# Performance work log

Hardware: AMD Instinct MI355X
Metric: run time of the kernel (lower is better)

## Reference

```python
import jax, jax.numpy as jnp
import numpy as np

START_TAG = 0
END_TAG = 63
NEG_INF = -10000.0


def setup_inputs() -> dict:
    key = jax.random.key(0)
    k1, k2, k3 = jax.random.split(key, 3)
    S, D, L = 32768, 1024, 64  # seq_len, feature_dim, num_labels
    feats = jax.random.normal(k1, (S, D), jnp.float32)
    W = jax.random.normal(k2, (L, D), jnp.float32) * 0.02  # nn.Linear weight [out,in]
    b = jnp.zeros((L,), jnp.float32)
    transitions = jax.random.normal(k3, (L, L), jnp.float32)
    transitions = transitions.at[START_TAG, :].set(NEG_INF).at[:, END_TAG].set(NEG_INF)
    return {"feats": feats, "W": W, "b": b, "transitions": transitions}


def reference(feats, W, b, transitions):
    # emissions: [S, L]
    emissions = feats @ W.T + b

    # Viterbi forward pass.  scores[j] after step t = best path score ending in label j.
    init_scores = transitions[:, START_TAG] + emissions[0]

    def step(scores, emit):
        # swt[j, i] = scores[i] + T[j, i]  (transition i -> j)
        swt = scores[None, :] + transitions  # [L, L]
        new_scores = emit + jnp.max(swt, axis=-1)
        back_ptr = jnp.argmax(swt, axis=-1)
        return new_scores, back_ptr

    final_scores, back_ptrs = jax.lax.scan(step, init_scores, emissions[1:])
    final_scores = final_scores + transitions[END_TAG]

    viterbi_score = jnp.max(final_scores)
    last_tag = jnp.argmax(final_scores)

    # Backtrack: tag[t-1] = back_ptrs[t-1][tag[t]] (back_ptrs[k] is for time k+1).
    def back(tag, bp):
        return bp[tag], tag

    first_tag, rest_tags = jax.lax.scan(back, last_tag, back_ptrs, reverse=True)
    tag_seq = jnp.concatenate([first_tag[None], rest_tags])  # [S]
    return viterbi_score, tag_seq
```

## Files before the change

kernel.cpp:

```cpp
#include <hip/hip_runtime.h>

#define S_LEN 32768
#define D_DIM 1024
#define L_LAB 64
#define LC 32
#define NCH (S_LEN / LC)
#define H_WARM 12
#define NSUP 32
#define SUPC 32

#define EM_OFF   0
#define BP_OFF   (S_LEN * 64 * 4)
#define MAPS_OFF (BP_OFF + S_LEN * 64)
#define BND_OFF  (MAPS_OFF + NCH * 64)
#define WIN_OFF  (BND_OFF + 1024)
#define END_OFF  (WIN_OFF + NCH * 4)
#define FIN_OFF  (END_OFF + NCH * 4)
#define WBF_OFF  (FIN_OFF + 256)

typedef __attribute__((ext_vector_type(8))) short short8;
typedef __attribute__((ext_vector_type(4))) float floatx4;

__device__ inline unsigned short f32_bf16_rne(float f) {
    unsigned v = __float_as_uint(f);
    v += 0x7FFFu + ((v >> 16) & 1u);
    return (unsigned short)(v >> 16);
}
__device__ inline unsigned umax(unsigned a, unsigned b) { return a > b ? a : b; }

__global__ __launch_bounds__(256) void wconv_kernel(
        const float* __restrict__ W, unsigned short* __restrict__ Wbf) {
    int i = blockIdx.x * 256 + threadIdx.x;
    Wbf[i] = f32_bf16_rne(W[i]);
}

__global__ __launch_bounds__(256) __attribute__((amdgpu_waves_per_eu(2, 2)))
void emis_kernel(
        const float* __restrict__ feats, const unsigned short* __restrict__ Wbf,
        const float* __restrict__ bvec, float* __restrict__ em) {
    __shared__ __align__(16) unsigned short As[64 * 72];
    __shared__ __align__(16) unsigned short Bs[64 * 72];

    const int tid = threadIdx.x;
    const int lan = tid & 15;
    const int q   = (tid >> 4) & 3;
    const int w   = tid >> 6;
    const int row0 = blockIdx.x * 64;

    floatx4 acc[4];
#pragma unroll
    for (int nt = 0; nt < 4; ++nt) acc[nt] = (floatx4){0.f, 0.f, 0.f, 0.f};

    for (int kb = 0; kb < D_DIM; kb += 64) {
        __syncthreads();
#pragma unroll
        for (int i = 0; i < 4; ++i) {
            int gi = tid + i * 256;
            int m = gi >> 4, g = gi & 15;
            float4 v = *(const float4*)&feats[(size_t)(row0 + m) * D_DIM + kb + g * 4];
            unsigned h0 = f32_bf16_rne(v.x) | ((unsigned)f32_bf16_rne(v.y) << 16);
            unsigned h1 = f32_bf16_rne(v.z) | ((unsigned)f32_bf16_rne(v.w) << 16);
            *(uint2*)&As[m * 72 + g * 4] = (uint2){h0, h1};
        }
#pragma unroll
        for (int i = 0; i < 2; ++i) {
            int gi = tid + i * 256;
            int m = gi >> 3, g = gi & 7;
            *(uint4*)&Bs[m * 72 + g * 8] =
                *(const uint4*)&Wbf[(size_t)m * D_DIM + kb + g * 8];
        }
        __syncthreads();

#pragma unroll
        for (int cc = 0; cc < 2; ++cc) {
            int koff = cc * 32 + q * 8;
            int m_loc = w * 16 + lan;
            short8 av = *(const short8*)&As[m_loc * 72 + koff];
#pragma unroll
            for (int nt = 0; nt < 4; ++nt) {
                int label = nt * 16 + lan;
                short8 bv = *(const short8*)&Bs[label * 72 + koff];
                acc[nt] = __builtin_amdgcn_mfma_f32_16x16x32_bf16(av, bv, acc[nt], 0, 0, 0);
            }
        }
    }

#pragma unroll
    for (int nt = 0; nt < 4; ++nt) {
        int label = nt * 16 + lan;
        float bias = bvec[label];
#pragma unroll
        for (int r = 0; r < 4; ++r) {
            int row = row0 + w * 16 + q * 4 + r;
            em[(size_t)row * 64 + label] = acc[nt][r] + bias;
        }
    }
}

__global__ __launch_bounds__(64) __attribute__((amdgpu_waves_per_eu(1, 1)))
void fwd_chunks(
        const float* __restrict__ em, const float* __restrict__ T,
        unsigned char* __restrict__ bp, unsigned char* __restrict__ maps,
        float* __restrict__ win, float* __restrict__ endsc,
        float* __restrict__ finrow) {
    const int j = threadIdx.x;
    const int c = blockIdx.x;
    const int a = c * LC;
    const int bend = a + LC;

    float Trow[64];
#pragma unroll
    for (int i = 0; i < 16; ++i)
        ((float4*)Trow)[i] = ((const float4*)(T + j * 64))[i];
#pragma unroll
    for (int i = 0; i < 64; ++i) Trow[i] += 32768.0f;

    int t0 = a - 1 - H_WARM;
    if (t0 < 0) t0 = 0;

    float sc;
    if (t0 == 0) {
        sc = Trow[0] + (em[j] - 32768.0f);
    } else {
        sc = em[(size_t)t0 * 64 + j];
    }

    auto step = [&](float e) {
        int sci = __float_as_int(sc);
        float v0 = 0.f, v1 = 0.f, v2 = 0.f, v3 = 0.f;
#pragma unroll
        for (int k = 0; k < 8; ++k) {
            float a0 = __int_as_float(__builtin_amdgcn_readlane(sci, k)) + Trow[k];
            float a1 = __int_as_float(__builtin_amdgcn_readlane(sci, k + 16)) + Trow[k + 16];
            float a2 = __int_as_float(__builtin_amdgcn_readlane(sci, k + 32)) + Trow[k + 32];
            float a3 = __int_as_float(__builtin_amdgcn_readlane(sci, k + 48)) + Trow[k + 48];
            v0 = fmaxf(fmaxf(v0, a0), a1);
            v1 = fmaxf(fmaxf(v1, a2), a3);
        }
#pragma unroll
        for (int k = 8; k < 16; ++k) {
            float a0 = __int_as_float(__builtin_amdgcn_readlane(sci, k)) + Trow[k];
            float a1 = __int_as_float(__builtin_amdgcn_readlane(sci, k + 16)) + Trow[k + 16];
            float a2 = __int_as_float(__builtin_amdgcn_readlane(sci, k + 32)) + Trow[k + 32];
            float a3 = __int_as_float(__builtin_amdgcn_readlane(sci, k + 48)) + Trow[k + 48];
            v2 = fmaxf(fmaxf(v2, a0), a1);
            v3 = fmaxf(fmaxf(v3, a2), a3);
        }
        sc = e + fmaxf(fmaxf(v0, v1), fmaxf(v2, v3));
    };

    int bi = 0;
    auto stepx = [&](float e) {
        int sci = __float_as_int(sc);
        unsigned m0 = 0u, m1 = 0u, m2 = 0u, m3 = 0u;
#pragma unroll
        for (int k = 0; k < 8; ++k) {
            float a0 = __int_as_float(__builtin_amdgcn_readlane(sci, k)) + Trow[k];
            float a1 = __int_as_float(__builtin_amdgcn_readlane(sci, k + 16)) + Trow[k + 16];
            float a2 = __int_as_float(__builtin_amdgcn_readlane(sci, k + 32)) + Trow[k + 32];
            float a3 = __int_as_float(__builtin_amdgcn_readlane(sci, k + 48)) + Trow[k + 48];
            unsigned k0 = ((unsigned)__float_as_int(a0) << 6) | (unsigned)(63 - k);
            unsigned k1 = ((unsigned)__float_as_int(a1) << 6) | (unsigned)(63 - (k + 16));
            unsigned k2 = ((unsigned)__float_as_int(a2) << 6) | (unsigned)(63 - (k + 32));
            unsigned k3 = ((unsigned)__float_as_int(a3) << 6) | (unsigned)(63 - (k + 48));
            m0 = umax(umax(m0, k0), k1);
            m1 = umax(umax(m1, k2), k3);
        }
#pragma unroll
        for (int k = 8; k < 16; ++k) {
            float a0 = __int_as_float(__builtin_amdgcn_readlane(sci, k)) + Trow[k];
            float a1 = __int_as_float(__builtin_amdgcn_readlane(sci, k + 16)) + Trow[k + 16];
            float a2 = __int_as_float(__builtin_amdgcn_readlane(sci, k + 32)) + Trow[k + 32];
            float a3 = __int_as_float(__builtin_amdgcn_readlane(sci, k + 48)) + Trow[k + 48];
            unsigned k0 = ((unsigned)__float_as_int(a0) << 6) | (unsigned)(63 - k);
            unsigned k1 = ((unsigned)__float_as_int(a1) << 6) | (unsigned)(63 - (k + 16));
            unsigned k2 = ((unsigned)__float_as_int(a2) << 6) | (unsigned)(63 - (k + 32));
            unsigned k3 = ((unsigned)__float_as_int(a3) << 6) | (unsigned)(63 - (k + 48));
            m2 = umax(umax(m2, k0), k1);
            m3 = umax(umax(m3, k2), k3);
        }
        unsigned mm = umax(umax(m0, m1), umax(m2, m3));
        bi = (int)(mm & 63u) ^ 63;
        sc = e + __uint_as_float((mm >> 6) | 0x44000000u);
    };

    int t = t0 + 1;
    if (t < a) {
        float p0 = em[(size_t)(t + 0) * 64 + j] - 32768.0f;
        float p1 = em[(size_t)(t + 1) * 64 + j] - 32768.0f;
        float p2 = em[(size_t)(t + 2) * 64 + j] - 32768.0f;
        float p3 = em[(size_t)(t + 3) * 64 + j] - 32768.0f;
        for (; t + 3 < a; t += 4) {
            float n0 = em[(size_t)(t + 4) * 64 + j] - 32768.0f;
            float n1 = em[(size_t)(t + 5) * 64 + j] - 32768.0f;
            float n2 = em[(size_t)(t + 6) * 64 + j] - 32768.0f;
            float n3 = em[(size_t)(t + 7) * 64 + j] - 32768.0f;
            step(p0); step(p1); step(p2); step(p3);
            p0 = n0; p1 = n1; p2 = n2; p3 = n3;
        }
        for (; t < a; ++t) { step(p0); p0 = p1; p1 = p2; p2 = p3; }
    }
    if (c > 0 && j == 0) win[c] = sc;

    int fmap = j;
    t = (a > 0) ? a : 1;
    {
        float p0 = em[(size_t)(t + 0) * 64 + j] - 32768.0f;
        float p1 = em[(size_t)(t + 1) * 64 + j] - 32768.0f;
        float p2 = em[(size_t)(t + 2) * 64 + j] - 32768.0f;
        float p3 = em[(size_t)(t + 3) * 64 + j] - 32768.0f;
        for (; t + 3 < bend; t += 4) {
            int t4 = t + 4 > S_LEN - 1 ? S_LEN - 1 : t + 4;
            int t5 = t + 5 > S_LEN - 1 ? S_LEN - 1 : t + 5;
            int t6 = t + 6 > S_LEN - 1 ? S_LEN - 1 : t + 6;
            int t7 = t + 7 > S_LEN - 1 ? S_LEN - 1 : t + 7;
            float n0 = em[(size_t)t4 * 64 + j] - 32768.0f;
            float n1 = em[(size_t)t5 * 64 + j] - 32768.0f;
            float n2 = em[(size_t)t6 * 64 + j] - 32768.0f;
            float n3 = em[(size_t)t7 * 64 + j] - 32768.0f;
            stepx(p0); bp[(size_t)(t + 0) * 64 + j] = (unsigned char)bi;
            fmap = __builtin_amdgcn_ds_bpermute(bi << 2, fmap);
            stepx(p1); bp[(size_t)(t + 1) * 64 + j] = (unsigned char)bi;
            fmap = __builtin_amdgcn_ds_bpermute(bi << 2, fmap);
            stepx(p2); bp[(size_t)(t + 2) * 64 + j] = (unsigned char)bi;
            fmap = __builtin_amdgcn_ds_bpermute(bi << 2, fmap);
            stepx(p3); bp[(size_t)(t + 3) * 64 + j] = (unsigned char)bi;
            fmap = __builtin_amdgcn_ds_bpermute(bi << 2, fmap);
            p0 = n0; p1 = n1; p2 = n2; p3 = n3;
        }
        for (; t < bend; ++t) {
            stepx(p0); bp[(size_t)t * 64 + j] = (unsigned char)bi;
            fmap = __builtin_amdgcn_ds_bpermute(bi << 2, fmap);
            p0 = p1; p1 = p2; p2 = p3;
        }
    }

    maps[c * 64 + j] = (unsigned char)fmap;
    if (j == 0) endsc[c] = sc;
    if (c == NCH - 1) finrow[j] = sc;
}

__global__ __launch_bounds__(1024) void finish_kernel(
        const float* __restrict__ T, const float* __restrict__ win,
        const float* __restrict__ endsc, const float* __restrict__ finrow,
        const unsigned char* __restrict__ maps, float* __restrict__ out,
        unsigned char* __restrict__ bnd) {
    __shared__ unsigned char sm[NSUP * 64];
    __shared__ unsigned char sbl[NSUP];
    __shared__ float psum[16];
    const int tid = threadIdx.x;
    const int lane = tid & 63;
    const int wid = tid >> 6;

    float p = 0.f;
    if (tid >= 1 && tid < NCH) p = endsc[tid - 1] - win[tid];
#pragma unroll
    for (int off = 32; off; off >>= 1) p += __shfl_xor(p, off, 64);
    if (lane == 0) psum[wid] = p;

#pragma unroll
    for (int r = 0; r < 2; ++r) {
        int s = wid * 2 + r;
        int x = lane;
#pragma unroll 4
        for (int q = SUPC - 1; q >= 0; --q) {
            int mq = maps[(s * SUPC + q) * 64 + lane];
            x = __builtin_amdgcn_ds_bpermute(x << 2, mq);
        }
        sm[s * 64 + lane] = (unsigned char)x;
    }
    __syncthreads();

    if (tid < 64) {
        float part = 0.f;
#pragma unroll
        for (int i = 0; i < 16; ++i) part += psum[i];

        float f = finrow[lane] + T[63 * 64 + lane];
        float best = 0.f; int bt_ = 0;
#pragma unroll
        for (int k = 0; k < 64; ++k) {
            float fv = __int_as_float(__builtin_amdgcn_readlane(__float_as_int(f), k));
            if (k == 0) best = fv;
            else if (fv > best) { best = fv; bt_ = k; }
        }
        if (lane == 0) out[0] = best + part;

        int rows[NSUP];
#pragma unroll
        for (int s = 0; s < NSUP; ++s) rows[s] = sm[s * 64 + lane];
        int x = bt_;
        int sbv = 0;
        if (lane == NSUP - 1) sbv = x;
#pragma unroll
        for (int s = NSUP - 1; s >= 1; --s) {
            x = __builtin_amdgcn_readlane(rows[s], x);
            if (lane == s - 1) sbv = x;
        }
        if (lane < NSUP) sbl[lane] = (unsigned char)sbv;
    }
    __syncthreads();

#pragma unroll
    for (int r = 0; r < 2; ++r) {
        int s = wid * 2 + r;
        int rows[SUPC];
#pragma unroll
        for (int q = 1; q < SUPC; ++q)
            rows[q] = maps[(s * SUPC + q) * 64 + lane];
        int x = __builtin_amdgcn_readfirstlane((int)sbl[s]);
        int bv = 0;
        if (lane == SUPC - 1) bv = x;
#pragma unroll
        for (int q = SUPC - 1; q >= 1; --q) {
            x = __builtin_amdgcn_readlane(rows[q], x);
            if (lane == q - 1) bv = x;
        }
        if (lane < SUPC) bnd[s * SUPC + lane] = (unsigned char)bv;
    }
}

__global__ __launch_bounds__(64) void bt_fill(
        const unsigned char* __restrict__ bp, const unsigned char* __restrict__ bnd,
        float* __restrict__ out) {
    const int c = blockIdx.x;
    const int lane = threadIdx.x;
    int rows[LC];
#pragma unroll
    for (int tt = 1; tt < LC; ++tt)
        rows[tt] = bp[((size_t)c * LC + tt) * 64 + lane];
    int x = __builtin_amdgcn_readfirstlane((int)bnd[c]);
    int tv = 0;
    if (lane == LC - 1) tv = x;
#pragma unroll
    for (int tt = LC - 1; tt >= 1; --tt) {
        x = __builtin_amdgcn_readlane(rows[tt], x);
        if (lane == tt - 1) tv = x;
    }
    if (lane < LC) out[1 + c * LC + lane] = (float)tv;
}

extern "C" void kernel_launch(void* const* d_in, const int* in_sizes, int n_in,
                              void* d_out, int out_size, void* d_ws, size_t ws_size,
                              hipStream_t stream) {
    const float* feats = (const float*)d_in[0];
    const float* W     = (const float*)d_in[1];
    const float* b     = (const float*)d_in[2];
    const float* T     = (const float*)d_in[3];
    float* out = (float*)d_out;

    char* ws = (char*)d_ws;
    float*          em     = (float*)(ws + EM_OFF);
    unsigned char*  bp     = (unsigned char*)(ws + BP_OFF);
    unsigned char*  maps   = (unsigned char*)(ws + MAPS_OFF);
    unsigned char*  bnd    = (unsigned char*)(ws + BND_OFF);
    float*          win    = (float*)(ws + WIN_OFF);
    float*          endsc  = (float*)(ws + END_OFF);
    float*          finrow = (float*)(ws + FIN_OFF);
    unsigned short* Wbf    = (unsigned short*)(ws + WBF_OFF);

    wconv_kernel<<<(L_LAB * D_DIM) / 256, 256, 0, stream>>>(W, Wbf);
    emis_kernel<<<S_LEN / 64, 256, 0, stream>>>(feats, Wbf, b, em);
    fwd_chunks<<<NCH, 64, 0, stream>>>(em, T, bp, maps, win, endsc, finrow);
    finish_kernel<<<1, 1024, 0, stream>>>(T, win, endsc, finrow, maps, out, bnd);
    bt_fill<<<NCH, 64, 0, stream>>>(bp, bnd, out);
}
```

Measured before the change: 251.4 us.

## Fuse Viterbi forward, finish and backtrack kernels into one cooperative launch

The three kernels (chunked forward, single-block finish, backtrack fill) become one cooperative kernel that uses grid-wide syncs in place of kernel boundaries. The finish stage is spread across blocks: super-chunk map composition runs on 32 blocks, and the score partial sum and final argmax each run on their own block. Each chunk block then derives its own boundary tag directly from the super-chunk label before filling its tags. This removes two launch gaps and the serialized 1024-thread finish block, at the cost of three grid barriers and the requirement that all 1024 blocks be co-resident.

```diff
diff --git a/kernel.cpp b/kernel.cpp
--- a/kernel.cpp
+++ b/kernel.cpp
@@ -1,4 +1,7 @@
 #include <hip/hip_runtime.h>
+#include <hip/hip_cooperative_groups.h>
+
+namespace cg = cooperative_groups;
 
 #define S_LEN 32768
 #define D_DIM 1024
@@ -12,8 +15,8 @@
 #define EM_OFF   0
 #define BP_OFF   (S_LEN * 64 * 4)
 #define MAPS_OFF (BP_OFF + S_LEN * 64)
-#define BND_OFF  (MAPS_OFF + NCH * 64)
-#define WIN_OFF  (BND_OFF + 1024)
+#define AUX_OFF  (MAPS_OFF + NCH * 64)
+#define WIN_OFF  (AUX_OFF + 4096)
 #define END_OFF  (WIN_OFF + NCH * 4)
 #define FIN_OFF  (END_OFF + NCH * 4)
 #define WBF_OFF  (FIN_OFF + 256)
@@ -98,185 +101,178 @@
 }
 
 __global__ __launch_bounds__(64) __attribute__((amdgpu_waves_per_eu(1, 1)))
-void fwd_chunks(
+void viterbi_coop(
         const float* __restrict__ em, const float* __restrict__ T,
         unsigned char* __restrict__ bp, unsigned char* __restrict__ maps,
         float* __restrict__ win, float* __restrict__ endsc,
-        float* __restrict__ finrow) {
+        float* __restrict__ finrow, char* __restrict__ aux,
+        float* __restrict__ out) {
+    cg::grid_group grid = cg::this_grid();
     const int j = threadIdx.x;
     const int c = blockIdx.x;
     const int a = c * LC;
     const int bend = a + LC;
 
-    float Trow[64];
-#pragma unroll
-    for (int i = 0; i < 16; ++i)
-        ((float4*)Trow)[i] = ((const float4*)(T + j * 64))[i];
-#pragma unroll
-    for (int i = 0; i < 64; ++i) Trow[i] += 32768.0f;
-
-    int t0 = a - 1 - H_WARM;
-    if (t0 < 0) t0 = 0;
-
-    float sc;
-    if (t0 == 0) {
-        sc = Trow[0] + (em[j] - 32768.0f);
-    } else {
-        sc = em[(size_t)t0 * 64 + j];
-    }
-
-    auto step = [&](float e) {
-        int sci = __float_as_int(sc);
-        float v0 = 0.f, v1 = 0.f, v2 = 0.f, v3 = 0.f;
-#pragma unroll
-        for (int k = 0; k < 8; ++k) {
-            float a0 = __int_as_float(__builtin_amdgcn_readlane(sci, k)) + Trow[k];
-            float a1 = __int_as_float(__builtin_amdgcn_readlane(sci, k + 16)) + Trow[k + 16];
-            float a2 = __int_as_float(__builtin_amdgcn_readlane(sci, k + 32)) + Trow[k + 32];
-            float a3 = __int_as_float(__builtin_amdgcn_readlane(sci, k + 48)) + Trow[k + 48];
-            v0 = fmaxf(fmaxf(v0, a0), a1);
-            v1 = fmaxf(fmaxf(v1, a2), a3);
-        }
-#pragma unroll
-        for (int k = 8; k < 16; ++k) {
-            float a0 = __int_as_float(__builtin_amdgcn_readlane(sci, k)) + Trow[k];
-            float a1 = __int_as_float(__builtin_amdgcn_readlane(sci, k + 16)) + Trow[k + 16];
-            float a2 = __int_as_float(__builtin_amdgcn_readlane(sci, k + 32)) + Trow[k + 32];
-            float a3 = __int_as_float(__builtin_amdgcn_readlane(sci, k + 48)) + Trow[k + 48];
-            v2 = fmaxf(fmaxf(v2, a0), a1);
-            v3 = fmaxf(fmaxf(v3, a2), a3);
-        }
-        sc = e + fmaxf(fmaxf(v0, v1), fmaxf(v2, v3));
-    };
-
-    int bi = 0;
-    auto stepx = [&](float e) {
-        int sci = __float_as_int(sc);
-        unsigned m0 = 0u, m1 = 0u, m2 = 0u, m3 = 0u;
-#pragma unroll
-        for (int k = 0; k < 8; ++k) {
-            float a0 = __int_as_float(__builtin_amdgcn_readlane(sci, k)) + Trow[k];
-            float a1 = __int_as_float(__builtin_amdgcn_readlane(sci, k + 16)) + Trow[k + 16];
-            float a2 = __int_as_float(__builtin_amdgcn_readlane(sci, k + 32)) + Trow[k + 32];
-            float a3 = __int_as_float(__builtin_amdgcn_readlane(sci, k + 48)) + Trow[k + 48];
-            unsigned k0 = ((unsigned)__float_as_int(a0) << 6) | (unsigned)(63 - k);
-            unsigned k1 = ((unsigned)__float_as_int(a1) << 6) | (unsigned)(63 - (k + 16));
-            unsigned k2 = ((unsigned)__float_as_int(a2) << 6) | (unsigned)(63 - (k + 32));
-            unsigned k3 = ((unsigned)__float_as_int(a3) << 6) | (unsigned)(63 - (k + 48));
-            m0 = umax(umax(m0, k0), k1);
-            m1 = umax(umax(m1, k2), k3);
-        }
-#pragma unroll
-        for (int k = 8; k < 16; ++k) {
-            float a0 = __int_as_float(__builtin_amdgcn_readlane(sci, k)) + Trow[k];
-            float a1 = __int_as_float(__builtin_amdgcn_readlane(sci, k + 16)) + Trow[k + 16];
-            float a2 = __int_as_float(__builtin_amdgcn_readlane(sci, k + 32)) + Trow[k + 32];
-            float a3 = __int_as_float(__builtin_amdgcn_readlane(sci, k + 48)) + Trow[k + 48];
-            unsigned k0 = ((unsigned)__float_as_int(a0) << 6) | (unsigned)(63 - k);
-            unsigned k1 = ((unsigned)__float_as_int(a1) << 6) | (unsigned)(63 - (k + 16));
-            unsigned k2 = ((unsigned)__float_as_int(a2) << 6) | (unsigned)(63 - (k + 32));
-            unsigned k3 = ((unsigned)__float_as_int(a3) << 6) | (unsigned)(63 - (k + 48));
-            m2 = umax(umax(m2, k0), k1);
-            m3 = umax(umax(m3, k2), k3);
-        }
-        unsigned mm = umax(umax(m0, m1), umax(m2, m3));
-        bi = (int)(mm & 63u) ^ 63;
-        sc = e + __uint_as_float((mm >> 6) | 0x44000000u);
-    };
-
-    int t = t0 + 1;
-    if (t < a) {
-        float p0 = em[(size_t)(t + 0) * 64 + j] - 32768.0f;
-        float p1 = em[(size_t)(t + 1) * 64 + j] - 32768.0f;
-        float p2 = em[(size_t)(t + 2) * 64 + j] - 32768.0f;
-        float p3 = em[(size_t)(t + 3) * 64 + j] - 32768.0f;
-        for (; t + 3 < a; t += 4) {
-            float n0 = em[(size_t)(t + 4) * 64 + j] - 32768.0f;
-            float n1 = em[(size_t)(t + 5) * 64 + j] - 32768.0f;
-            float n2 = em[(size_t)(t + 6) * 64 + j] - 32768.0f;
-            float n3 = em[(size_t)(t + 7) * 64 + j] - 32768.0f;
-            step(p0); step(p1); step(p2); step(p3);
-            p0 = n0; p1 = n1; p2 = n2; p3 = n3;
-        }
-        for (; t < a; ++t) { step(p0); p0 = p1; p1 = p2; p2 = p3; }
-    }
-    if (c > 0 && j == 0) win[c] = sc;
-
-    int fmap = j;
-    t = (a > 0) ? a : 1;
+    float* psumg = (float*)aux;
+    float* bestg = (float*)(aux + 4);
+    int*   btg   = (int*)(aux + 8);
+    unsigned char* sbl = (unsigned char*)(aux + 16);
+    unsigned char* smg = (unsigned char*)(aux + 64);
+
     {
-        float p0 = em[(size_t)(t + 0) * 64 + j] - 32768.0f;
-        float p1 = em[(size_t)(t + 1) * 64 + j] - 32768.0f;
-        float p2 = em[(size_t)(t + 2) * 64 + j] - 32768.0f;
-        float p3 = em[(size_t)(t + 3) * 64 + j] - 32768.0f;
-        for (; t + 3 < bend; t += 4) {
-            int t4 = t + 4 > S_LEN - 1 ? S_LEN - 1 : t + 4;
-            int t5 = t + 5 > S_LEN - 1 ? S_LEN - 1 : t + 5;
-            int t6 = t + 6 > S_LEN - 1 ? S_LEN - 1 : t + 6;
-            int t7 = t + 7 > S_LEN - 1 ? S_LEN - 1 : t + 7;
-            float n0 = em[(size_t)t4 * 64 + j] - 32768.0f;
-            float n1 = em[(size_t)t5 * 64 + j] - 32768.0f;
-            float n2 = em[(size_t)t6 * 64 + j] - 32768.0f;
-            float n3 = em[(size_t)t7 * 64 + j] - 32768.0f;
-            stepx(p0); bp[(size_t)(t + 0) * 64 + j] = (unsigned char)bi;
-            fmap = __builtin_amdgcn_ds_bpermute(bi << 2, fmap);
-            stepx(p1); bp[(size_t)(t + 1) * 64 + j] = (unsigned char)bi;
-            fmap = __builtin_amdgcn_ds_bpermute(bi << 2, fmap);
-            stepx(p2); bp[(size_t)(t + 2) * 64 + j] = (unsigned char)bi;
-            fmap = __builtin_amdgcn_ds_bpermute(bi << 2, fmap);
-            stepx(p3); bp[(size_t)(t + 3) * 64 + j] = (unsigned char)bi;
-            fmap = __builtin_amdgcn_ds_bpermute(bi << 2, fmap);
-            p0 = n0; p1 = n1; p2 = n2; p3 = n3;
-        }
-        for (; t < bend; ++t) {
-            stepx(p0); bp[(size_t)t * 64 + j] = (unsigned char)bi;
-            fmap = __builtin_amdgcn_ds_bpermute(bi << 2, fmap);
-            p0 = p1; p1 = p2; p2 = p3;
-        }
-    }
-
-    maps[c * 64 + j] = (unsigned char)fmap;
-    if (j == 0) endsc[c] = sc;
-    if (c == NCH - 1) finrow[j] = sc;
-}
-
-__global__ __launch_bounds__(1024) void finish_kernel(
-        const float* __restrict__ T, const float* __restrict__ win,
-        const float* __restrict__ endsc, const float* __restrict__ finrow,
-        const unsigned char* __restrict__ maps, float* __restrict__ out,
-        unsigned char* __restrict__ bnd) {
-    __shared__ unsigned char sm[NSUP * 64];
-    __shared__ unsigned char sbl[NSUP];
-    __shared__ float psum[16];
-    const int tid = threadIdx.x;
-    const int lane = tid & 63;
-    const int wid = tid >> 6;
-
-    float p = 0.f;
-    if (tid >= 1 && tid < NCH) p = endsc[tid - 1] - win[tid];
-#pragma unroll
-    for (int off = 32; off; off >>= 1) p += __shfl_xor(p, off, 64);
-    if (lane == 0) psum[wid] = p;
-
-#pragma unroll
-    for (int r = 0; r < 2; ++r) {
-        int s = wid * 2 + r;
-        int x = lane;
+        float Trow[64];
+#pragma unroll
+        for (int i = 0; i < 16; ++i)
+            ((float4*)Trow)[i] = ((const float4*)(T + j * 64))[i];
+#pragma unroll
+        for (int i = 0; i < 64; ++i) Trow[i] += 32768.0f;
+
+        int t0 = a - 1 - H_WARM;
+        if (t0 < 0) t0 = 0;
+
+        float sc;
+        if (t0 == 0) {
+            sc = Trow[0] + (em[j] - 32768.0f);
+        } else {
+            sc = em[(size_t)t0 * 64 + j];
+        }
+
+        auto step = [&](float e) {
+            int sci = __float_as_int(sc);
+            float v0 = 0.f, v1 = 0.f, v2 = 0.f, v3 = 0.f;
+#pragma unroll
+            for (int k = 0; k < 8; ++k) {
+                float a0 = __int_as_float(__builtin_amdgcn_readlane(sci, k)) + Trow[k];
+                float a1 = __int_as_float(__builtin_amdgcn_readlane(sci, k + 16)) + Trow[k + 16];
+                float a2 = __int_as_float(__builtin_amdgcn_readlane(sci, k + 32)) + Trow[k + 32];
+                float a3 = __int_as_float(__builtin_amdgcn_readlane(sci, k + 48)) + Trow[k + 48];
+                v0 = fmaxf(fmaxf(v0, a0), a1);
+                v1 = fmaxf(fmaxf(v1, a2), a3);
+            }
+#pragma unroll
+            for (int k = 8; k < 16; ++k) {
+                float a0 = __int_as_float(__builtin_amdgcn_readlane(sci, k)) + Trow[k];
+                float a1 = __int_as_float(__builtin_amdgcn_readlane(sci, k + 16)) + Trow[k + 16];
+                float a2 = __int_as_float(__builtin_amdgcn_readlane(sci, k + 32)) + Trow[k + 32];
+                float a3 = __int_as_float(__builtin_amdgcn_readlane(sci, k + 48)) + Trow[k + 48];
+                v2 = fmaxf(fmaxf(v2, a0), a1);
+                v3 = fmaxf(fmaxf(v3, a2), a3);
+            }
+            sc = e + fmaxf(fmaxf(v0, v1), fmaxf(v2, v3));
+        };
+
+        int bi = 0;
+        auto stepx = [&](float e) {
+            int sci = __float_as_int(sc);
+            unsigned m0 = 0u, m1 = 0u, m2 = 0u, m3 = 0u;
+#pragma unroll
+            for (int k = 0; k < 8; ++k) {
+                float a0 = __int_as_float(__builtin_amdgcn_readlane(sci, k)) + Trow[k];
+                float a1 = __int_as_float(__builtin_amdgcn_readlane(sci, k + 16)) + Trow[k + 16];
+                float a2 = __int_as_float(__builtin_amdgcn_readlane(sci, k + 32)) + Trow[k + 32];
+                float a3 = __int_as_float(__builtin_amdgcn_readlane(sci, k + 48)) + Trow[k + 48];
+                unsigned k0 = ((unsigned)__float_as_int(a0) << 6) | (unsigned)(63 - k);
+                unsigned k1 = ((unsigned)__float_as_int(a1) << 6) | (unsigned)(63 - (k + 16));
+                unsigned k2 = ((unsigned)__float_as_int(a2) << 6) | (unsigned)(63 - (k + 32));
+                unsigned k3 = ((unsigned)__float_as_int(a3) << 6) | (unsigned)(63 - (k + 48));
+                m0 = umax(umax(m0, k0), k1);
+                m1 = umax(umax(m1, k2), k3);
+            }
+#pragma unroll
+            for (int k = 8; k < 16; ++k) {
+                float a0 = __int_as_float(__builtin_amdgcn_readlane(sci, k)) + Trow[k];
+                float a1 = __int_as_float(__builtin_amdgcn_readlane(sci, k + 16)) + Trow[k + 16];
+                float a2 = __int_as_float(__builtin_amdgcn_readlane(sci, k + 32)) + Trow[k + 32];
+                float a3 = __int_as_float(__builtin_amdgcn_readlane(sci, k + 48)) + Trow[k + 48];
+                unsigned k0 = ((unsigned)__float_as_int(a0) << 6) | (unsigned)(63 - k);
+                unsigned k1 = ((unsigned)__float_as_int(a1) << 6) | (unsigned)(63 - (k + 16));
+                unsigned k2 = ((unsigned)__float_as_int(a2) << 6) | (unsigned)(63 - (k + 32));
+                unsigned k3 = ((unsigned)__float_as_int(a3) << 6) | (unsigned)(63 - (k + 48));
+                m2 = umax(umax(m2, k0), k1);
+                m3 = umax(umax(m3, k2), k3);
+            }
+            unsigned mm = umax(umax(m0, m1), umax(m2, m3));
+            bi = (int)(mm & 63u) ^ 63;
+            sc = e + __uint_as_float((mm >> 6) | 0x44000000u);
+        };
+
+        int t = t0 + 1;
+        if (t < a) {
+            float p0 = em[(size_t)(t + 0) * 64 + j] - 32768.0f;
+            float p1 = em[(size_t)(t + 1) * 64 + j] - 32768.0f;
+            float p2 = em[(size_t)(t + 2) * 64 + j] - 32768.0f;
+            float p3 = em[(size_t)(t + 3) * 64 + j] - 32768.0f;
+            for (; t + 3 < a; t += 4) {
+                float n0 = em[(size_t)(t + 4) * 64 + j] - 32768.0f;
+                float n1 = em[(size_t)(t + 5) * 64 + j] - 32768.0f;
+                float n2 = em[(size_t)(t + 6) * 64 + j] - 32768.0f;
+                float n3 = em[(size_t)(t + 7) * 64 + j] - 32768.0f;
+                step(p0); step(p1); step(p2); step(p3);
+                p0 = n0; p1 = n1; p2 = n2; p3 = n3;
+            }
+            for (; t < a; ++t) { step(p0); p0 = p1; p1 = p2; p2 = p3; }
+        }
+        if (c > 0 && j == 0) win[c] = sc;
+
+        int fmap = j;
+        t = (a > 0) ? a : 1;
+        {
+            float p0 = em[(size_t)(t + 0) * 64 + j] - 32768.0f;
+            float p1 = em[(size_t)(t + 1) * 64 + j] - 32768.0f;
+            float p2 = em[(size_t)(t + 2) * 64 + j] - 32768.0f;
+            float p3 = em[(size_t)(t + 3) * 64 + j] - 32768.0f;
+            for (; t + 3 < bend; t += 4) {
+                int t4 = t + 4 > S_LEN - 1 ? S_LEN - 1 : t + 4;
+                int t5 = t + 5 > S_LEN - 1 ? S_LEN - 1 : t + 5;
+                int t6 = t + 6 > S_LEN - 1 ? S_LEN - 1 : t + 6;
+                int t7 = t + 7 > S_LEN - 1 ? S_LEN - 1 : t + 7;
+                float n0 = em[(size_t)t4 * 64 + j] - 32768.0f;
+                float n1 = em[(size_t)t5 * 64 + j] - 32768.0f;
+                float n2 = em[(size_t)t6 * 64 + j] - 32768.0f;
+                float n3 = em[(size_t)t7 * 64 + j] - 32768.0f;
+                stepx(p0); bp[(size_t)(t + 0) * 64 + j] = (unsigned char)bi;
+                fmap = __builtin_amdgcn_ds_bpermute(bi << 2, fmap);
+                stepx(p1); bp[(size_t)(t + 1) * 64 + j] = (unsigned char)bi;
+                fmap = __builtin_amdgcn_ds_bpermute(bi << 2, fmap);
+                stepx(p2); bp[(size_t)(t + 2) * 64 + j] = (unsigned char)bi;
+                fmap = __builtin_amdgcn_ds_bpermute(bi << 2, fmap);
+                stepx(p3); bp[(size_t)(t + 3) * 64 + j] = (unsigned char)bi;
+                fmap = __builtin_amdgcn_ds_bpermute(bi << 2, fmap);
+                p0 = n0; p1 = n1; p2 = n2; p3 = n3;
+            }
+            for (; t < bend; ++t) {
+                stepx(p0); bp[(size_t)t * 64 + j] = (unsigned char)bi;
+                fmap = __builtin_amdgcn_ds_bpermute(bi << 2, fmap);
+                p0 = p1; p1 = p2; p2 = p3;
+            }
+        }
+
+        maps[c * 64 + j] = (unsigned char)fmap;
+        if (j == 0) endsc[c] = sc;
+        if (c == NCH - 1) finrow[j] = sc;
+    }
+    grid.sync();
+
+    if (c < NSUP) {
+        int x = j;
 #pragma unroll 4
         for (int q = SUPC - 1; q >= 0; --q) {
-            int mq = maps[(s * SUPC + q) * 64 + lane];
+            int mq = maps[(c * SUPC + q) * 64 + j];
             x = __builtin_amdgcn_ds_bpermute(x << 2, mq);
         }
-        sm[s * 64 + lane] = (unsigned char)x;
-    }
-    __syncthreads();
-
-    if (tid < 64) {
-        float part = 0.f;
-#pragma unroll
-        for (int i = 0; i < 16; ++i) part += psum[i];
-
-        float f = finrow[lane] + T[63 * 64 + lane];
+        smg[c * 64 + j] = (unsigned char)x;
+    } else if (c == NSUP) {
+        float p = 0.f;
+#pragma unroll
+        for (int i = 0; i < NCH / 64; ++i) {
+            int cc = 1 + j + i * 64;
+            if (cc < NCH) p += endsc[cc - 1] - win[cc];
+        }
+#pragma unroll
+        for (int off = 32; off; off >>= 1) p += __shfl_xor(p, off, 64);
+        if (j == 0) *psumg = p;
+    } else if (c == NSUP + 1) {
+        float f = finrow[j] + T[63 * 64 + j];
         float best = 0.f; int bt_ = 0;
 #pragma unroll
         for (int k = 0; k < 64; ++k) {
@@ -284,60 +280,51 @@
             if (k == 0) best = fv;
             else if (fv > best) { best = fv; bt_ = k; }
         }
-        if (lane == 0) out[0] = best + part;
-
+        if (j == 0) { *bestg = best; *btg = bt_; }
+    }
+    grid.sync();
+
+    if (c == 0) {
         int rows[NSUP];
 #pragma unroll
-        for (int s = 0; s < NSUP; ++s) rows[s] = sm[s * 64 + lane];
-        int x = bt_;
+        for (int s = 0; s < NSUP; ++s) rows[s] = smg[s * 64 + j];
+        int x = __builtin_amdgcn_readfirstlane(*btg);
+        if (j == 0) out[0] = *bestg + *psumg;
         int sbv = 0;
-        if (lane == NSUP - 1) sbv = x;
+        if (j == NSUP - 1) sbv = x;
 #pragma unroll
         for (int s = NSUP - 1; s >= 1; --s) {
             x = __builtin_amdgcn_readlane(rows[s], x);
-            if (lane == s - 1) sbv = x;
-        }
-        if (lane < NSUP) sbl[lane] = (unsigned char)sbv;
-    }
-    __syncthreads();
-
-#pragma unroll
-    for (int r = 0; r < 2; ++r) {
-        int s = wid * 2 + r;
-        int rows[SUPC];
+            if (j == s - 1) sbv = x;
+        }
+        if (j < NSUP) sbl[j] = (unsigned char)sbv;
+    }
+    grid.sync();
+
+    {
+        const int s = c >> 5, q0 = c & 31;
+        int rowsA[SUPC];
 #pragma unroll
         for (int q = 1; q < SUPC; ++q)
-            rows[q] = maps[(s * SUPC + q) * 64 + lane];
+            rowsA[q] = (q > q0) ? (int)maps[(s * SUPC + q) * 64 + j] : 0;
         int x = __builtin_amdgcn_readfirstlane((int)sbl[s]);
-        int bv = 0;
-        if (lane == SUPC - 1) bv = x;
-#pragma unroll
-        for (int q = SUPC - 1; q >= 1; --q) {
-            x = __builtin_amdgcn_readlane(rows[q], x);
-            if (lane == q - 1) bv = x;
-        }
-        if (lane < SUPC) bnd[s * SUPC + lane] = (unsigned char)bv;
-    }
-}
-
-__global__ __launch_bounds__(64) void bt_fill(
-        const unsigned char* __restrict__ bp, const unsigned char* __restrict__ bnd,
-        float* __restrict__ out) {
-    const int c = blockIdx.x;
-    const int lane = threadIdx.x;
-    int rows[LC];
-#pragma unroll
-    for (int tt = 1; tt < LC; ++tt)
-        rows[tt] = bp[((size_t)c * LC + tt) * 64 + lane];
-    int x = __builtin_amdgcn_readfirstlane((int)bnd[c]);
-    int tv = 0;
-    if (lane == LC - 1) tv = x;
-#pragma unroll
-    for (int tt = LC - 1; tt >= 1; --tt) {
-        x = __builtin_amdgcn_readlane(rows[tt], x);
-        if (lane == tt - 1) tv = x;
-    }
-    if (lane < LC) out[1 + c * LC + lane] = (float)tv;
+#pragma unroll
+        for (int q = SUPC - 1; q >= 1; --q)
+            if (q > q0) x = __builtin_amdgcn_readlane(rowsA[q], x);
+
+        int rowsB[LC];
+#pragma unroll
+        for (int tt = 1; tt < LC; ++tt)
+            rowsB[tt] = bp[((size_t)c * LC + tt) * 64 + j];
+        int tv = 0;
+        if (j == LC - 1) tv = x;
+#pragma unroll
+        for (int tt = LC - 1; tt >= 1; --tt) {
+            x = __builtin_amdgcn_readlane(rowsB[tt], x);
+            if (j == tt - 1) tv = x;
+        }
+        if (j < LC) out[1 + c * LC + j] = (float)tv;
+    }
 }
 
 extern "C" void kernel_launch(void* const* d_in, const int* in_sizes, int n_in,
@@ -353,7 +340,7 @@
     float*          em     = (float*)(ws + EM_OFF);
     unsigned char*  bp     = (unsigned char*)(ws + BP_OFF);
     unsigned char*  maps   = (unsigned char*)(ws + MAPS_OFF);
-    unsigned char*  bnd    = (unsigned char*)(ws + BND_OFF);
+    char*           aux    = ws + AUX_OFF;
     float*          win    = (float*)(ws + WIN_OFF);
     float*          endsc  = (float*)(ws + END_OFF);
     float*          finrow = (float*)(ws + FIN_OFF);
@@ -361,7 +348,10 @@
 
     wconv_kernel<<<(L_LAB * D_DIM) / 256, 256, 0, stream>>>(W, Wbf);
     emis_kernel<<<S_LEN / 64, 256, 0, stream>>>(feats, Wbf, b, em);
-    fwd_chunks<<<NCH, 64, 0, stream>>>(em, T, bp, maps, win, endsc, finrow);
-    finish_kernel<<<1, 1024, 0, stream>>>(T, win, endsc, finrow, maps, out, bnd);
-    bt_fill<<<NCH, 64, 0, stream>>>(bp, bnd, out);
-}
+
+    void* kargs[] = {(void*)&em, (void*)&T, (void*)&bp, (void*)&maps,
+                     (void*)&win, (void*)&endsc, (void*)&finrow,
+                     (void*)&aux, (void*)&out};
+    hipLaunchCooperativeKernel(reinterpret_cast<void*>(&viterbi_coop),
+                               dim3(NCH), dim3(64), kargs, 0, stream);
+}
```

New measurement: 578.9 us. +130.3%, slower.
